# Optimization experiments

Measured on AMD Instinct MI355X. Metric: run time of the kernel, lower is better.

The kernel has to match this reference:

```python
import jax, jax.numpy as jnp
import numpy as np

B, S, D, H = 4, 1024, 1024, 16
HS = D // H  # head_size = 64


def setup_inputs() -> dict:
    key = jax.random.key(0)
    ks = jax.random.split(key, 6)
    scale = 1.0 / np.sqrt(D)
    data = jax.random.normal(ks[0], (B, S, D), dtype=jnp.float32)
    # Per-head projection weights, stacked: [H, D, HS] (no bias, per nn.Linear(bias=False))
    Wq = jax.random.normal(ks[1], (H, D, HS), dtype=jnp.float32) * scale
    Wk = jax.random.normal(ks[2], (H, D, HS), dtype=jnp.float32) * scale
    Wv = jax.random.normal(ks[3], (H, D, HS), dtype=jnp.float32) * scale
    # Output projection: [H*HS, D] plus bias [D]
    Wo = jax.random.normal(ks[4], (H * HS, D), dtype=jnp.float32) * scale
    bo = jax.random.normal(ks[5], (D,), dtype=jnp.float32) * 0.01
    return {"data": data, "Wq": Wq, "Wk": Wk, "Wv": Wv, "Wo": Wo, "bo": bo}


def reference(data, Wq, Wk, Wv, Wo, bo):
    b, s, d = data.shape
    # Per-head Q/K/V projections (self-attention: encoder_data = data)
    q = jnp.einsum('bsd,hde->bhse', data, Wq)  # [B,H,S,HS]
    k = jnp.einsum('bsd,hde->bhse', data, Wk)
    v = jnp.einsum('bsd,hde->bhse', data, Wv)
    # NOTE: original scales by sqrt(embedding_dimension), not sqrt(head_size)
    scores = jnp.einsum('bhse,bhte->bhst', q, k) / jnp.sqrt(jnp.asarray(d, dtype=data.dtype))
    # causal mask (tril of block_size, sliced to [S, S])
    causal = jnp.tril(jnp.ones((s, s), dtype=bool))
    scores = jnp.where(causal, scores, -jnp.inf)
    attn = jax.nn.softmax(scores, axis=-1)  # dropout rate 0.0 -> identity
    out = jnp.einsum('bhst,bhte->bhse', attn, v)  # [B,H,S,HS]
    # concat heads along feature dim (head order matches ModuleList order)
    out = out.transpose(0, 2, 1, 3).reshape(b, s, -1)  # [B,S,H*HS]
    return out @ Wo + bo
```

## Files before the change

### kernel.cpp

```cpp
#include <hip/hip_runtime.h>
#include <hip/hip_bf16.h>
#include <stdint.h>

#define NEG_SENTINEL (-1e30f)

typedef short s16x8 __attribute__((ext_vector_type(8)));
typedef float f32x4 __attribute__((ext_vector_type(4)));

__device__ __forceinline__ ushort f2bf(float f) {
  union { float f; uint32_t u; } v; v.f = f;
  uint32_t u = v.u;
  u += 0x7fffu + ((u >> 16) & 1u);
  return (ushort)(u >> 16);
}
__device__ __forceinline__ ushort f2bf_rn(float f) {
  union { float f; uint32_t u; } v; v.f = f;
  return (ushort)((v.u + 0x8000u) >> 16);
}

__device__ __forceinline__ void async_ld16(ushort* lds, const ushort* g) {
  __builtin_amdgcn_global_load_lds(
      (const __attribute__((address_space(1))) uint32_t*)g,
      (__attribute__((address_space(3))) uint32_t*)lds, 16, 0, 0);
}

__global__ __launch_bounds__(256) void convert_f32_bf16(
    const float* __restrict__ src, ushort* __restrict__ dst) {
  long i = ((long)blockIdx.x * 256 + threadIdx.x) * 8;
  float4 a = *(const float4*)(src + i);
  float4 b = *(const float4*)(src + i + 4);
  union { ushort u[8]; uint4 v; } o;
  o.u[0] = f2bf(a.x); o.u[1] = f2bf(a.y); o.u[2] = f2bf(a.z); o.u[3] = f2bf(a.w);
  o.u[4] = f2bf(b.x); o.u[5] = f2bf(b.y); o.u[6] = f2bf(b.z); o.u[7] = f2bf(b.w);
  *(uint4*)(dst + i) = o.v;
}

__global__ __launch_bounds__(256) void transpose_w3(
    const float* __restrict__ Wq, const float* __restrict__ Wk,
    const float* __restrict__ Wv, ushort* __restrict__ WTall) {
  const int z = blockIdx.z;
  const int matsel = z >> 4;
  const float* src = (matsel == 0 ? Wq : (matsel == 1 ? Wk : Wv)) +
                     (long)(z & 15) * 65536;
  ushort* dst = WTall + (long)z * 65536;
  const int it = blockIdx.y;
  __shared__ __align__(16) ushort tile[64 * 72];
  const int tid = threadIdx.x;
#pragma unroll
  for (int p = 0; p < 4; ++p) {
    int chunk = tid + p * 256;
    int r = chunk >> 4, c0 = (chunk & 15) * 4;
    float4 f = *(const float4*)(src + (long)(it * 64 + r) * 64 + c0);
    union { ushort u[4]; uint2 v; } o;
    o.u[0] = f2bf(f.x); o.u[1] = f2bf(f.y); o.u[2] = f2bf(f.z); o.u[3] = f2bf(f.w);
    *(uint2*)&tile[r * 72 + c0] = o.v;
  }
  __syncthreads();
#pragma unroll
  for (int p = 0; p < 2; ++p) {
    int chunk = tid + p * 256;
    int r = chunk >> 3, c0 = (chunk & 7) * 8;
    union { ushort u[8]; uint4 v; } tmp;
#pragma unroll
    for (int k2 = 0; k2 < 8; ++k2) tmp.u[k2] = tile[(c0 + k2) * 72 + r];
    *(uint4*)(dst + (long)r * 1024 + it * 64 + c0) = tmp.v;
  }
}

__global__ __launch_bounds__(256) void transpose_cvt(
    const float* __restrict__ src, ushort* __restrict__ dst) {
  const int jt = blockIdx.x;
  const int it = blockIdx.y;
  __shared__ __align__(16) ushort tile[64 * 72];
  const int tid = threadIdx.x;
#pragma unroll
  for (int p = 0; p < 4; ++p) {
    int chunk = tid + p * 256;
    int r = chunk >> 4, c0 = (chunk & 15) * 4;
    float4 f = *(const float4*)(src + (long)(it * 64 + r) * 1024 + jt * 64 + c0);
    union { ushort u[4]; uint2 v; } o;
    o.u[0] = f2bf(f.x); o.u[1] = f2bf(f.y); o.u[2] = f2bf(f.z); o.u[3] = f2bf(f.w);
    *(uint2*)&tile[r * 72 + c0] = o.v;
  }
  __syncthreads();
#pragma unroll
  for (int p = 0; p < 2; ++p) {
    int chunk = tid + p * 256;
    int r = chunk >> 3, c0 = (chunk & 7) * 8;
    union { ushort u[8]; uint4 v; } tmp;
#pragma unroll
    for (int k2 = 0; k2 < 8; ++k2) tmp.u[k2] = tile[(c0 + k2) * 72 + r];
    *(uint4*)(dst + (long)(jt * 64 + r) * 1024 + it * 64 + c0) = tmp.v;
  }
}

__device__ __forceinline__ void gemm_core_128x128(
    const ushort* __restrict__ A, const ushort* __restrict__ BT,
    ushort* As, ushort* Bs, f32x4 acc[4][4]) {
  const int tid = threadIdx.x;
  const int lane = tid & 63, w = tid >> 6, quad = lane >> 4, l15 = lane & 15;
  const int wm = w >> 1, wn = w & 1;
  for (int k0 = 0; k0 < 1024; k0 += 64) {
#pragma unroll
    for (int p = 0; p < 4; ++p) {
      int c = tid + p * 256;
      int r = c >> 3, c8 = (c & 7) * 8;
      async_ld16(As + c * 8, A + (long)r * 1024 + k0 + c8);
      async_ld16(Bs + c * 8, BT + (long)r * 1024 + k0 + c8);
    }
    __syncthreads();
#pragma unroll
    for (int kk = 0; kk < 64; kk += 32) {
      s16x8 af[4], bfr[4];
#pragma unroll
      for (int mi = 0; mi < 4; ++mi)
        af[mi] = *(const s16x8*)&As[(wm * 64 + mi * 16 + l15) * 64 + kk + quad * 8];
#pragma unroll
      for (int ni = 0; ni < 4; ++ni)
        bfr[ni] = *(const s16x8*)&Bs[(wn * 64 + ni * 16 + l15) * 64 + kk + quad * 8];
#pragma unroll
      for (int mi = 0; mi < 4; ++mi)
#pragma unroll
        for (int ni = 0; ni < 4; ++ni)
          acc[mi][ni] = __builtin_amdgcn_mfma_f32_16x16x32_bf16(
              af[mi], bfr[ni], acc[mi][ni], 0, 0, 0);
    }
    __syncthreads();
  }
}

#define BAR() do { asm volatile("" ::: "memory"); \
  __builtin_amdgcn_s_barrier(); \
  asm volatile("" ::: "memory"); } while (0)
#define LGKM0() do { asm volatile("s_waitcnt lgkmcnt(0)" ::: "memory"); \
  __builtin_amdgcn_sched_barrier(0); } while (0)
#define STAGE2(LDSB, G) do { \
  async_ld16((LDSB) + o0, (G) + so0); \
  async_ld16((LDSB) + o0 + 4096, (G) + so0 + 65536); } while (0)
#define LD_A(PA, MIB) do { \
  _Pragma("unroll") for (int dm = 0; dm < 4; ++dm) { \
    afr[dm][0] = *(const s16x8*)((PA) + ((MIB) + dm) * 1024); \
    afr[dm][1] = *(const s16x8*)((PA) + ((MIB) + dm) * 1024 + 512); } } while (0)
#define LD_B(PB, NIB) do { \
  _Pragma("unroll") for (int dn = 0; dn < 2; ++dn) { \
    bfr[(NIB) + dn][0] = *(const s16x8*)((PB) + ((NIB) + dn) * 1024); \
    bfr[(NIB) + dn][1] = *(const s16x8*)((PB) + ((NIB) + dn) * 1024 + 512); } } while (0)
#define MFMA_Q(MIB, NIB) do { \
  __builtin_amdgcn_s_setprio(1); \
  _Pragma("unroll") for (int kg = 0; kg < 2; ++kg) \
    _Pragma("unroll") for (int dm = 0; dm < 4; ++dm) \
      _Pragma("unroll") for (int dn = 0; dn < 2; ++dn) \
        acc[(MIB) + dm][(NIB) + dn] = __builtin_amdgcn_mfma_f32_16x16x32_bf16( \
            afr[dm][kg], bfr[(NIB) + dn][kg], acc[(MIB) + dm][(NIB) + dn], 0, 0, 0); \
  __builtin_amdgcn_s_setprio(0); } while (0)

__global__ __launch_bounds__(512, 2) void qkv_proj256(
    const ushort* __restrict__ dataB, const ushort* __restrict__ WTall,
    ushort* __restrict__ QKV) {
  __shared__ __align__(16) ushort smem[65536];
  const int tid = threadIdx.x;
  const int lane = tid & 63, w = tid >> 6, quad = lane >> 4, l15 = lane & 15;
  const int wm = w >> 2, wn = w & 3;
  const int m0 = blockIdx.x * 256;
  const int n0 = blockIdx.y * 256;

  const int o0 = tid * 8;
  {
  }
  const int st_ = o0 >> 9, u_ = o0 & 511;
  const int u0_ = u_ ^ (((u_ >> 8) & 1) << 4);
  const long so0 = (long)((st_ >> 1) * 16 + (u0_ >> 5)) * 1024 +
                   (st_ & 1) * 32 + (u0_ & 31);

  const ushort* Ab = dataB + (long)m0 * 1024;
  const ushort* Bb = WTall + (long)n0 * 1024;

  const int alane = (l15 * 32 + quad * 8) ^ (((l15 >> 3) & 1) << 4);
  const ushort* pA0 = smem + wm * 8192 + alane;
  const ushort* pB0 = smem + 16384 + (wn >> 1) * 8192 + (wn & 1) * 4096 + alane;
  const ushort* pA1 = pA0 + 32768;
  const ushort* pB1 = pB0 + 32768;

  f32x4 acc[8][4];
  const f32x4 z = {0.f, 0.f, 0.f, 0.f};
#pragma unroll
  for (int mi = 0; mi < 8; ++mi)
#pragma unroll
    for (int ni = 0; ni < 4; ++ni) acc[mi][ni] = z;

  s16x8 afr[4][2];
  s16x8 bfr[4][2];

  STAGE2(smem + 16384, Bb);
  STAGE2(smem + 16384 + 8192, Bb + 131072);
  STAGE2(smem, Ab);
  STAGE2(smem + 8192, Ab + 131072);
  STAGE2(smem + 32768 + 16384, Bb + 64);
  STAGE2(smem + 32768 + 16384 + 8192, Bb + 131072 + 64);
  asm volatile("s_waitcnt vmcnt(4)" ::: "memory");
  BAR();

#pragma unroll 1
  for (int it = 0; it < 8; ++it) {
    const int t0k = it * 128;
    const bool sN = (it < 7);
    LD_A(pA0, 0); LD_B(pB0, 0);
    STAGE2(smem + 32768, Ab + t0k + 64);
    asm volatile("s_waitcnt lgkmcnt(8)" ::: "memory");
    BAR(); LGKM0();
    MFMA_Q(0, 0);
    BAR();
    LD_B(pB0, 2);
    STAGE2(smem + 32768 + 8192, Ab + 131072 + t0k + 64);
    BAR(); LGKM0();
    MFMA_Q(0, 2);
    BAR();
    LD_A(pA0, 4);
    if (sN) STAGE2(smem + 16384, Bb + t0k + 128);
    BAR(); LGKM0();
    MFMA_Q(4, 0);
    BAR();
    if (sN) STAGE2(smem + 16384 + 8192, Bb + 131072 + t0k + 128);
    BAR(); LGKM0();
    MFMA_Q(4, 2);
    if (sN) { asm volatile("s_waitcnt vmcnt(4)" ::: "memory"); }
    else    { asm volatile("s_waitcnt vmcnt(0)" ::: "memory"); }
    BAR();
    LD_A(pA1, 0); LD_B(pB1, 0);
    if (sN) STAGE2(smem, Ab + t0k + 128);
    asm volatile("s_waitcnt lgkmcnt(8)" ::: "memory");
    BAR(); LGKM0();
    MFMA_Q(0, 0);
    BAR();
    LD_B(pB1, 2);
    if (sN) STAGE2(smem + 8192, Ab + 131072 + t0k + 128);
    BAR(); LGKM0();
    MFMA_Q(0, 2);
    BAR();
    LD_A(pA1, 4);
    if (sN) STAGE2(smem + 32768 + 16384, Bb + t0k + 192);
    BAR(); LGKM0();
    MFMA_Q(4, 0);
    BAR();
    if (sN) STAGE2(smem + 32768 + 16384 + 8192, Bb + 131072 + t0k + 192);
    BAR(); LGKM0();
    MFMA_Q(4, 2);
    if (sN) {
      asm volatile("s_waitcnt vmcnt(4)" ::: "memory");
      BAR();
    }
  }

  const int matsel = n0 >> 10;
  const int bI = m0 >> 10, s0 = m0 & 1023;
  const int nloc0 = (n0 & 1023) + wn * 64;
  if (matsel < 2) {
    const float sc = (matsel == 0) ? 0.03125f : 1.0f;
    ushort* base = QKV + (long)matsel * 4194304 + (long)bI * 1048576;
#pragma unroll
    for (int mi = 0; mi < 8; ++mi) {
#pragma unroll
      for (int ni = 0; ni < 4; ++ni) {
        int n = nloc0 + ni * 16 + l15;
        int h = n >> 6, e = n & 63;
        ushort* col = base + (long)h * 65536 + e;
        int sb = s0 + wm * 128 + mi * 16 + quad * 4;
#pragma unroll
        for (int i = 0; i < 4; ++i)
          col[(long)(sb + i) * 64] = f2bf(acc[mi][ni][i] * sc);
      }
    }
  } else {
    ushort* base = QKV + 8388608 + (long)bI * 1048576;
#pragma unroll
    for (int mi = 0; mi < 8; ++mi) {
#pragma unroll
      for (int ni = 0; ni < 4; ++ni) {
        int n = nloc0 + ni * 16 + l15;
        int h = n >> 6, e = n & 63;
        int sb = s0 + wm * 128 + mi * 16 + quad * 4;
        union { ushort u[4]; uint2 v; } o;
#pragma unroll
        for (int i = 0; i < 4; ++i) o.u[i] = f2bf(acc[mi][ni][i]);
        *(uint2*)(base + (long)h * 65536 + (long)e * 1024 + sb) = o.v;
      }
    }
  }
}

__global__ __launch_bounds__(256) void out_proj(
    const ushort* __restrict__ Ocat, const ushort* __restrict__ WoT,
    const float* __restrict__ bo, float* __restrict__ out) {
  __shared__ __align__(16) ushort As[128 * 64];
  __shared__ __align__(16) ushort Bs[128 * 64];
  const int m0 = blockIdx.x * 128;
  const int n0 = blockIdx.y * 128;
  f32x4 acc[4][4];
  const f32x4 z = {0.f, 0.f, 0.f, 0.f};
#pragma unroll
  for (int mi = 0; mi < 4; ++mi)
#pragma unroll
    for (int ni = 0; ni < 4; ++ni) acc[mi][ni] = z;
  gemm_core_128x128(Ocat + (long)m0 * 1024, WoT + (long)n0 * 1024, As, Bs, acc);

  const int tid = threadIdx.x;
  const int lane = tid & 63, w = tid >> 6, quad = lane >> 4, l15 = lane & 15;
  const int wm = w >> 1, wn = w & 1;
#pragma unroll
  for (int mi = 0; mi < 4; ++mi) {
#pragma unroll
    for (int ni = 0; ni < 4; ++ni) {
#pragma unroll
      for (int i = 0; i < 4; ++i) {
        int m = m0 + wm * 64 + mi * 16 + quad * 4 + i;
        int n = n0 + wn * 64 + ni * 16 + l15;
        out[(long)m * 1024 + n] = acc[mi][ni][i] + bo[n];
      }
    }
  }
}

__global__ __launch_bounds__(512, 4) void attn_kernel(
    const ushort* __restrict__ QKV, ushort* __restrict__ Ocat) {
  __shared__ __align__(16) ushort Ks[128 * 72];
  __shared__ __align__(16) ushort Vs[64 * 136];
  __shared__ __align__(16) ushort Ps[8 * 16 * 136];
  const int qt = 7 - blockIdx.y;
  const int bh = blockIdx.x;
  const int b = bh >> 4, h = bh & 15;
  const int tid = threadIdx.x;
  const int w = tid >> 6, lane = tid & 63, quad = lane >> 4, l15 = lane & 15;
  const int q0 = qt * 128;

  const ushort* Qp = QKV + (long)bh * 65536;
  const ushort* Kp = QKV + 4194304 + (long)bh * 65536;
  const ushort* VTp = QKV + 8388608 + (long)bh * 65536;

  const int qrow = q0 + w * 16 + l15;
  s16x8 qf0 = *(const s16x8*)(Qp + (long)qrow * 64 + quad * 8);
  s16x8 qf1 = *(const s16x8*)(Qp + (long)qrow * 64 + 32 + quad * 8);

  f32x4 oacc[4];
  const f32x4 z = {0.f, 0.f, 0.f, 0.f};
#pragma unroll
  for (int et = 0; et < 4; ++et) oacc[et] = z;
  float l_i[4] = {0.f, 0.f, 0.f, 0.f};

  ushort* Psw = Ps + w * (16 * 136);
  const int nj = qt + 1;

  for (int j = 0; j < nj; ++j) {
#pragma unroll
    for (int p = 0; p < 2; ++p) {
      int c = tid + p * 512;
      { int r = c >> 3, c8 = (c & 7) * 8;
        *(uint4*)&Ks[r * 72 + c8] = *(const uint4*)(Kp + (long)(j * 128 + r) * 64 + c8); }
      { int r = c >> 4, c8 = (c & 15) * 8;
        *(uint4*)&Vs[r * 136 + c8] = *(const uint4*)(VTp + (long)r * 1024 + j * 128 + c8); }
    }
    __syncthreads();

    f32x4 sacc[8];
#pragma unroll
    for (int nt = 0; nt < 8; ++nt) sacc[nt] = z;
#pragma unroll
    for (int kk = 0; kk < 64; kk += 32) {
      s16x8 a = kk ? qf1 : qf0;
#pragma unroll
      for (int nt = 0; nt < 8; ++nt) {
        s16x8 bfr = *(const s16x8*)&Ks[(nt * 16 + l15) * 72 + kk + quad * 8];
        sacc[nt] = __builtin_amdgcn_mfma_f32_16x16x32_bf16(a, bfr, sacc[nt], 0, 0, 0);
      }
    }

    if (j == qt) {
      const int srow = q0 + w * 16 + quad * 4;
#pragma unroll
      for (int nt = 0; nt < 8; ++nt) {
#pragma unroll
        for (int i = 0; i < 4; ++i) {
          int tg = j * 128 + nt * 16 + l15;
          if (tg > srow + i) sacc[nt][i] = NEG_SENTINEL;
        }
      }
    }

#pragma unroll
    for (int i = 0; i < 4; ++i) {
#pragma unroll
      for (int nt = 0; nt < 8; ++nt) {
        float p = __expf(sacc[nt][i]);
        Psw[(quad * 4 + i) * 136 + nt * 16 + l15] = f2bf_rn(p);
        l_i[i] += p;
      }
    }

#pragma unroll
    for (int kk = 0; kk < 128; kk += 32) {
      s16x8 pa = *(const s16x8*)&Psw[l15 * 136 + kk + quad * 8];
#pragma unroll
      for (int et = 0; et < 4; ++et) {
        s16x8 vb = *(const s16x8*)&Vs[(et * 16 + l15) * 136 + kk + quad * 8];
        oacc[et] = __builtin_amdgcn_mfma_f32_16x16x32_bf16(pa, vb, oacc[et], 0, 0, 0);
      }
    }
    __syncthreads();
  }

#pragma unroll
  for (int i = 0; i < 4; ++i) {
#pragma unroll
    for (int d = 1; d < 16; d <<= 1) l_i[i] += __shfl_xor(l_i[i], d, 64);
  }

  ushort* Ob = Ocat + ((long)(b * 1024 + q0 + w * 16) * 1024) + h * 64;
#pragma unroll
  for (int et = 0; et < 4; ++et) {
#pragma unroll
    for (int i = 0; i < 4; ++i) {
      float denom = l_i[i];
      float v = oacc[et][i] / (denom > 0.f ? denom : 1.0f);
      Ob[(long)(quad * 4 + i) * 1024 + et * 16 + l15] = f2bf_rn(v);
    }
  }
}

extern "C" void kernel_launch(void* const* d_in, const int* in_sizes, int n_in,
                              void* d_out, int out_size, void* d_ws, size_t ws_size,
                              hipStream_t stream) {
  const float* data = (const float*)d_in[0];
  const float* Wq = (const float*)d_in[1];
  const float* Wk = (const float*)d_in[2];
  const float* Wv = (const float*)d_in[3];
  const float* Wo = (const float*)d_in[4];
  const float* bo = (const float*)d_in[5];
  float* out = (float*)d_out;

  ushort* ws = (ushort*)d_ws;
  ushort* QKV = ws;
  ushort* dataB = ws + 12582912;
  ushort* Ocat = ws + 16777216;
  ushort* WTall = ws + 20971520;
  ushort* WoT = ws + 20971520 + 3145728;

  dim3 blk(256);
  convert_f32_bf16<<<dim3(2048), blk, 0, stream>>>(data, dataB);
  transpose_w3<<<dim3(1, 16, 48), blk, 0, stream>>>(Wq, Wk, Wv, WTall);
  transpose_cvt<<<dim3(16, 16), blk, 0, stream>>>(Wo, WoT);
  qkv_proj256<<<dim3(16, 12), dim3(512), 0, stream>>>(dataB, WTall, QKV);
  attn_kernel<<<dim3(64, 8), dim3(512), 0, stream>>>(QKV, Ocat);
  out_proj<<<dim3(32, 8), blk, 0, stream>>>(Ocat, WoT, bo, out);
}
```

Measured before the change: 175.7 us.

## Rewrite attention as register-only per-wave 32x32 MFMA kernel with prefetch

Each wave now owns a 32-row query chunk of one (batch, head) pair and streams K and V^T straight from global memory into registers with one-step prefetch. It drops the shared-memory staging, the block barriers and the LDS round trip for P. It uses 32x32x16 MFMAs with K as the A operand, so the scores come out transposed and P can be fed to the PV MFMA via a cross-half lane shuffle. exp2f replaces __expf, with log2(e) folded into the Q scale, and the grid is ordered to launch long causal chunks first. The cost is redundant global or L2 reads of K and V per wave and less reuse across waves, in exchange for finer causal work granularity.

```diff
diff --git a/kernel.cpp b/kernel.cpp
--- a/kernel.cpp
+++ b/kernel.cpp
@@ -6,6 +6,7 @@
 
 typedef short s16x8 __attribute__((ext_vector_type(8)));
 typedef float f32x4 __attribute__((ext_vector_type(4)));
+typedef float f32x16 __attribute__((ext_vector_type(16)));
 
 __device__ __forceinline__ ushort f2bf(float f) {
   union { float f; uint32_t u; } v; v.f = f;
@@ -16,6 +17,12 @@
 __device__ __forceinline__ ushort f2bf_rn(float f) {
   union { float f; uint32_t u; } v; v.f = f;
   return (ushort)((v.u + 0x8000u) >> 16);
+}
+
+__device__ __forceinline__ uint32_t pk_bf16(float lo, float hi) {
+  uint32_t r;
+  asm("v_cvt_pk_bf16_f32 %0, %1, %2" : "=v"(r) : "v"(lo), "v"(hi));
+  return r;
 }
 
 __device__ __forceinline__ void async_ld16(ushort* lds, const ushort* g) {
@@ -165,8 +172,6 @@
   const int n0 = blockIdx.y * 256;
 
   const int o0 = tid * 8;
-  {
-  }
   const int st_ = o0 >> 9, u_ = o0 & 511;
   const int u0_ = u_ ^ (((u_ >> 8) & 1) << 4);
   const long so0 = (long)((st_ >> 1) * 16 + (u0_ >> 5)) * 1024 +
@@ -255,7 +260,7 @@
   const int bI = m0 >> 10, s0 = m0 & 1023;
   const int nloc0 = (n0 & 1023) + wn * 64;
   if (matsel < 2) {
-    const float sc = (matsel == 0) ? 0.03125f : 1.0f;
+    const float sc = (matsel == 0) ? 0.04508422f : 1.0f;
     ushort* base = QKV + (long)matsel * 4194304 + (long)bI * 1048576;
 #pragma unroll
     for (int mi = 0; mi < 8; ++mi) {
@@ -320,108 +325,106 @@
   }
 }
 
-__global__ __launch_bounds__(512, 4) void attn_kernel(
+__global__ __launch_bounds__(256, 2) void attn_kernel(
     const ushort* __restrict__ QKV, ushort* __restrict__ Ocat) {
-  __shared__ __align__(16) ushort Ks[128 * 72];
-  __shared__ __align__(16) ushort Vs[64 * 136];
-  __shared__ __align__(16) ushort Ps[8 * 16 * 136];
-  const int qt = 7 - blockIdx.y;
-  const int bh = blockIdx.x;
+  const int x = blockIdx.x;
+  const int tid = threadIdx.x;
+  const int w = tid >> 6;
+  const int lane = tid & 63, l31 = lane & 31, hi = lane >> 5;
+  const int c = (x < 256) ? (31 - (x >> 4)) : ((x - 256) >> 4);
+  const int bh = (x & 15) * 4 + w;
   const int b = bh >> 4, h = bh & 15;
-  const int tid = threadIdx.x;
-  const int w = tid >> 6, lane = tid & 63, quad = lane >> 4, l15 = lane & 15;
-  const int q0 = qt * 128;
+  const int q0 = c * 32;
 
   const ushort* Qp = QKV + (long)bh * 65536;
   const ushort* Kp = QKV + 4194304 + (long)bh * 65536;
   const ushort* VTp = QKV + 8388608 + (long)bh * 65536;
 
-  const int qrow = q0 + w * 16 + l15;
-  s16x8 qf0 = *(const s16x8*)(Qp + (long)qrow * 64 + quad * 8);
-  s16x8 qf1 = *(const s16x8*)(Qp + (long)qrow * 64 + 32 + quad * 8);
-
-  f32x4 oacc[4];
-  const f32x4 z = {0.f, 0.f, 0.f, 0.f};
-#pragma unroll
-  for (int et = 0; et < 4; ++et) oacc[et] = z;
-  float l_i[4] = {0.f, 0.f, 0.f, 0.f};
-
-  ushort* Psw = Ps + w * (16 * 136);
-  const int nj = qt + 1;
-
-  for (int j = 0; j < nj; ++j) {
-#pragma unroll
-    for (int p = 0; p < 2; ++p) {
-      int c = tid + p * 512;
-      { int r = c >> 3, c8 = (c & 7) * 8;
-        *(uint4*)&Ks[r * 72 + c8] = *(const uint4*)(Kp + (long)(j * 128 + r) * 64 + c8); }
-      { int r = c >> 4, c8 = (c & 15) * 8;
-        *(uint4*)&Vs[r * 136 + c8] = *(const uint4*)(VTp + (long)r * 1024 + j * 128 + c8); }
-    }
-    __syncthreads();
-
-    f32x4 sacc[8];
-#pragma unroll
-    for (int nt = 0; nt < 8; ++nt) sacc[nt] = z;
-#pragma unroll
-    for (int kk = 0; kk < 64; kk += 32) {
-      s16x8 a = kk ? qf1 : qf0;
-#pragma unroll
-      for (int nt = 0; nt < 8; ++nt) {
-        s16x8 bfr = *(const s16x8*)&Ks[(nt * 16 + l15) * 72 + kk + quad * 8];
-        sacc[nt] = __builtin_amdgcn_mfma_f32_16x16x32_bf16(a, bfr, sacc[nt], 0, 0, 0);
+  s16x8 qf[4];
+#pragma unroll
+  for (int es = 0; es < 4; ++es)
+    qf[es] = *(const s16x8*)(Qp + (long)(q0 + l31) * 64 + es * 16 + hi * 8);
+
+  f32x16 oacc0, oacc1;
+#pragma unroll
+  for (int r = 0; r < 16; ++r) { oacc0[r] = 0.f; oacc1[r] = 0.f; }
+  float l_part = 0.f;
+  const int nsub = c + 1;
+
+  s16x8 kc[4], vc[4], kn[4], vn[4];
+#pragma unroll
+  for (int es = 0; es < 4; ++es)
+    kc[es] = *(const s16x8*)(Kp + (long)l31 * 64 + es * 16 + hi * 8);
+#pragma unroll
+  for (int t = 0; t < 4; ++t)
+    vc[t] = *(const s16x8*)(VTp + (long)((t & 1) * 32 + l31) * 1024 +
+                            (t >> 1) * 16 + hi * 8);
+
+  for (int s = 0;; ++s) {
+    const bool last = (s + 1 >= nsub);
+    if (!last) {
+#pragma unroll
+      for (int es = 0; es < 4; ++es)
+        kn[es] = *(const s16x8*)(Kp + (long)((s + 1) * 32 + l31) * 64 +
+                                 es * 16 + hi * 8);
+#pragma unroll
+      for (int t = 0; t < 4; ++t)
+        vn[t] = *(const s16x8*)(VTp + (long)((t & 1) * 32 + l31) * 1024 +
+                                (s + 1) * 32 + (t >> 1) * 16 + hi * 8);
+    }
+    f32x16 sacc;
+#pragma unroll
+    for (int r = 0; r < 16; ++r) sacc[r] = 0.f;
+#pragma unroll
+    for (int es = 0; es < 4; ++es)
+      sacc = __builtin_amdgcn_mfma_f32_32x32x16_bf16(kc[es], qf[es], sacc,
+                                                     0, 0, 0);
+    if (s == c) {
+#pragma unroll
+      for (int r = 0; r < 16; ++r) {
+        int kvoff = (r & 3) + 8 * (r >> 2) + 4 * hi;
+        if (kvoff > l31) sacc[r] = NEG_SENTINEL;
       }
     }
-
-    if (j == qt) {
-      const int srow = q0 + w * 16 + quad * 4;
-#pragma unroll
-      for (int nt = 0; nt < 8; ++nt) {
-#pragma unroll
-        for (int i = 0; i < 4; ++i) {
-          int tg = j * 128 + nt * 16 + l15;
-          if (tg > srow + i) sacc[nt][i] = NEG_SENTINEL;
-        }
-      }
-    }
-
-#pragma unroll
-    for (int i = 0; i < 4; ++i) {
-#pragma unroll
-      for (int nt = 0; nt < 8; ++nt) {
-        float p = __expf(sacc[nt][i]);
-        Psw[(quad * 4 + i) * 136 + nt * 16 + l15] = f2bf_rn(p);
-        l_i[i] += p;
-      }
-    }
-
-#pragma unroll
-    for (int kk = 0; kk < 128; kk += 32) {
-      s16x8 pa = *(const s16x8*)&Psw[l15 * 136 + kk + quad * 8];
-#pragma unroll
-      for (int et = 0; et < 4; ++et) {
-        s16x8 vb = *(const s16x8*)&Vs[(et * 16 + l15) * 136 + kk + quad * 8];
-        oacc[et] = __builtin_amdgcn_mfma_f32_16x16x32_bf16(pa, vb, oacc[et], 0, 0, 0);
-      }
-    }
-    __syncthreads();
-  }
-
-#pragma unroll
-  for (int i = 0; i < 4; ++i) {
-#pragma unroll
-    for (int d = 1; d < 16; d <<= 1) l_i[i] += __shfl_xor(l_i[i], d, 64);
-  }
-
-  ushort* Ob = Ocat + ((long)(b * 1024 + q0 + w * 16) * 1024) + h * 64;
-#pragma unroll
-  for (int et = 0; et < 4; ++et) {
-#pragma unroll
-    for (int i = 0; i < 4; ++i) {
-      float denom = l_i[i];
-      float v = oacc[et][i] / (denom > 0.f ? denom : 1.0f);
-      Ob[(long)(quad * 4 + i) * 1024 + et * 16 + l15] = f2bf_rn(v);
-    }
+    float ex[16];
+#pragma unroll
+    for (int r = 0; r < 16; ++r) { ex[r] = exp2f(sacc[r]); l_part += ex[r]; }
+    uint32_t xw[8], yw[8];
+#pragma unroll
+    for (int k = 0; k < 8; ++k) xw[k] = pk_bf16(ex[2 * k], ex[2 * k + 1]);
+#pragma unroll
+    for (int k = 0; k < 8; ++k)
+      yw[k] = (uint32_t)__shfl_xor((int)xw[k], 32, 64);
+#pragma unroll
+    for (int win = 0; win < 2; ++win) {
+      const int bs = 4 * win;
+      union { uint32_t u[4]; s16x8 v; } pa;
+      pa.u[0] = hi ? yw[bs + 2] : xw[bs + 0];
+      pa.u[1] = hi ? yw[bs + 3] : xw[bs + 1];
+      pa.u[2] = hi ? xw[bs + 2] : yw[bs + 0];
+      pa.u[3] = hi ? xw[bs + 3] : yw[bs + 1];
+      oacc0 = __builtin_amdgcn_mfma_f32_32x32x16_bf16(pa.v, vc[win * 2 + 0],
+                                                      oacc0, 0, 0, 0);
+      oacc1 = __builtin_amdgcn_mfma_f32_32x32x16_bf16(pa.v, vc[win * 2 + 1],
+                                                      oacc1, 0, 0, 0);
+    }
+    if (last) break;
+#pragma unroll
+    for (int es = 0; es < 4; ++es) kc[es] = kn[es];
+#pragma unroll
+    for (int t = 0; t < 4; ++t) vc[t] = vn[t];
+  }
+
+  float l_tot = l_part + __shfl_xor(l_part, 32, 64);
+
+  ushort* Ob = Ocat + ((long)(b * 1024 + q0) * 1024) + h * 64;
+#pragma unroll
+  for (int r = 0; r < 16; ++r) {
+    int qloc = (r & 3) + 8 * (r >> 2) + 4 * hi;
+    float lv = __shfl(l_tot, qloc, 64);
+    float linv = __builtin_amdgcn_rcpf(lv > 1e-30f ? lv : 1.0f);
+    Ob[(long)qloc * 1024 + l31] = f2bf_rn(oacc0[r] * linv);
+    Ob[(long)qloc * 1024 + 32 + l31] = f2bf_rn(oacc1[r] * linv);
   }
 }
 
@@ -448,6 +451,6 @@
   transpose_w3<<<dim3(1, 16, 48), blk, 0, stream>>>(Wq, Wk, Wv, WTall);
   transpose_cvt<<<dim3(16, 16), blk, 0, stream>>>(Wo, WoT);
   qkv_proj256<<<dim3(16, 12), dim3(512), 0, stream>>>(dataB, WTall, QKV);
-  attn_kernel<<<dim3(64, 8), dim3(512), 0, stream>>>(QKV, Ocat);
+  attn_kernel<<<dim3(512), dim3(256), 0, stream>>>(QKV, Ocat);
   out_proj<<<dim3(32, 8), blk, 0, stream>>>(Ocat, WoT, bo, out);
 }
```

Result: slower. 183.5 us (+4.4%).
